# Kernel tuning notes

Measured on AMD Instinct MI355X. Metric: run time of the kernel, lower is better.

Reference implementation:

```python
import jax, jax.numpy as jnp
import numpy as np

B, T, S, H, D = 2, 2048, 2048, 16, 64
E = H * D  # embed_dim = 1024


def setup_inputs() -> dict:
    key = jax.random.key(0)
    k1, k2, k3, k4 = jax.random.split(key, 4)
    q = jax.random.normal(k1, (B, T, H, D), jnp.float32)
    kv = jax.random.normal(k2, (B, S, 2, H, D), jnp.float32)
    # nn.MultiheadAttention packed in-projection (xavier-ish scale) and out-projection
    in_proj_w = jax.random.normal(k3, (3 * E, E), jnp.float32) * (1.0 / np.sqrt(E)).astype(np.float32)
    in_proj_b = jnp.zeros((3 * E,), jnp.float32)
    out_proj_w = jax.random.normal(k4, (E, E), jnp.float32) * (1.0 / np.sqrt(E)).astype(np.float32)
    out_proj_b = jnp.zeros((E,), jnp.float32)
    return {"q": q, "kv": kv, "in_proj_w": in_proj_w, "in_proj_b": in_proj_b,
            "out_proj_w": out_proj_w, "out_proj_b": out_proj_b}


def reference(q, kv, in_proj_w, in_proj_b, out_proj_w, out_proj_b):
    Bq, Tq, Hh, Dd = q.shape
    Ss = kv.shape[1]
    Ee = Hh * Dd
    # flatten heads: q -> (B,T,E); kv unbinds k (two=0) and v (two=1)
    qf = q.reshape(Bq, Tq, Ee)
    kf = kv[:, :, 0].reshape(Bq, Ss, Ee)
    vf = kv[:, :, 1].reshape(Bq, Ss, Ee)
    wq, wk, wv = jnp.split(in_proj_w, 3, axis=0)
    bq, bk, bv = jnp.split(in_proj_b, 3)
    qp = (qf @ wq.T + bq).reshape(Bq, Tq, Hh, Dd).transpose(0, 2, 1, 3)  # bhtd
    kp = (kf @ wk.T + bk).reshape(Bq, Ss, Hh, Dd).transpose(0, 2, 1, 3)  # bhsd
    vp = (vf @ wv.T + bv).reshape(Bq, Ss, Hh, Dd).transpose(0, 2, 1, 3)  # bhsd
    scale = 1.0 / jnp.sqrt(jnp.asarray(Dd, qp.dtype))
    scores = jnp.einsum('bhtd,bhsd->bhts', qp, kp) * scale
    attn = jax.nn.softmax(scores, axis=-1)  # full SxS materialization, as in non-fused MHA
    ctx = jnp.einsum('bhts,bhsd->bhtd', attn, vp)
    ctx = ctx.transpose(0, 2, 1, 3).reshape(Bq, Tq, Ee)
    out = (ctx @ out_proj_w.T + out_proj_b).reshape(Bq, Tq, Hh, Dd)
    # need_weights=True default: weights averaged over heads -> (B,T,S)
    attn_weights = attn.mean(axis=1)
    return out, attn_weights
```

## Files before the change

kernel.cpp:

```cpp
#include <hip/hip_runtime.h>
#include <math.h>

#define Bb 2
#define Tt 2048
#define Ssz 2048
#define Hh 16
#define Dd 64
#define Ee 1024

#define NQ  (Bb*Tt*Ee)
#define NKV (Bb*Ssz*Ee)
#define NW  (3*Ee*Ee)
#define NWO (Ee*Ee)

#define LOG2E 1.44269504088896f

typedef __bf16 bf16x8 __attribute__((ext_vector_type(8)));
typedef float  floatx4 __attribute__((ext_vector_type(4)));
typedef unsigned short u16;
typedef unsigned int   u32;

__device__ __forceinline__ u16 f2bf(float f) {
    __bf16 h = (__bf16)f;
    union { __bf16 h; u16 u; } v; v.h = h; return v.u;
}
__device__ __forceinline__ float bf2f(u16 b) {
    union { u32 u; float f; } v; v.u = ((u32)b) << 16; return v.f;
}
__device__ __forceinline__ float load_f(const void* p, int i, bool isbf) {
    if (isbf) return bf2f(((const u16*)p)[i]);
    return ((const float*)p)[i];
}
__device__ __forceinline__ u32 load2(const void* p, int i, bool isbf) {
    if (isbf) return ((const u32*)p)[i >> 1];
    float2 f = ((const float2*)p)[i >> 1];
    return (u32)f2bf(f.x) | ((u32)f2bf(f.y) << 16);
}

typedef __attribute__((address_space(1))) const unsigned int gas_u32;
typedef __attribute__((address_space(3))) unsigned int las_u32;
__device__ __forceinline__ void gl_lds16(const u16* g, u16* l) {
    __builtin_amdgcn_global_load_lds((gas_u32*)g, (las_u32*)l, 16, 0, 0);
}

__device__ __forceinline__ int swz(int k, int row) {
    return (k & ~63) | ((((k >> 3) ^ row) & 7) << 3) | (k & 7);
}

__global__ void k_detect(const u32* __restrict__ qw, int* __restrict__ flag) {
    __shared__ int cnt;
    if (threadIdx.x == 0) cnt = 0;
    __syncthreads();
    int h = 0;
    for (int i = threadIdx.x; i < 4096; i += 256) {
        u32 w = qw[i];
        u32 b = (w >> 8) & 0x7Fu;
        if ((b & 0x7Cu) == 0x3Cu) h++;
    }
    atomicAdd(&cnt, h);
    __syncthreads();
    if (threadIdx.x == 0) flag[0] = (cnt > 2048) ? 1 : 0;
}

__global__ void k_pack(const void* __restrict__ q, const void* __restrict__ kv,
                       const void* __restrict__ w_in, const void* __restrict__ b_in,
                       const void* __restrict__ w_out, const void* __restrict__ b_out,
                       const int* __restrict__ flag,
                       u32* __restrict__ qb, u32* __restrict__ kb, u32* __restrict__ vb,
                       u32* __restrict__ wb, u32* __restrict__ wob, float* __restrict__ biases) {
    bool isbf = flag[0] != 0;
    int i = (blockIdx.x * 256 + threadIdx.x) * 2;
    if (i < NQ) { int row = i >> 10, k = i & 1023;
        qb[(((size_t)row << 10) | (u32)swz(k, row)) >> 1] = load2(q, i, isbf); return; }
    i -= NQ;
    if (i < NKV) { int row = i >> 10, e = i & 1023;
        kb[(((size_t)row << 10) | (u32)swz(e, row)) >> 1] = load2(kv, row*2048 + e, isbf); return; }
    i -= NKV;
    if (i < NKV) { int row = i >> 10, e = i & 1023;
        vb[(((size_t)row << 10) | (u32)swz(e, row)) >> 1] = load2(kv, row*2048 + 1024 + e, isbf); return; }
    i -= NKV;
    if (i < NW) { int row = i >> 10, k = i & 1023;
        wb[(((size_t)row << 10) | (u32)swz(k, row)) >> 1] = load2(w_in, i, isbf); return; }
    i -= NW;
    if (i < NWO) { int row = i >> 10, k = i & 1023;
        wob[(((size_t)row << 10) | (u32)swz(k, row)) >> 1] = load2(w_out, i, isbf); return; }
    i -= NWO;
    if (i < 3072) { biases[i] = load_f(b_in, i, isbf); biases[i+1] = load_f(b_in, i+1, isbf); return; }
    i -= 3072;
    if (i < 1024) { biases[3072+i] = load_f(b_out, i, isbf); biases[3072+i+1] = load_f(b_out, i+1, isbf); }
}

__device__ __forceinline__ void gemm128(const u16* __restrict__ Ab, const u16* __restrict__ Wb,
                                        u16* As, u16* Ws, floatx4 (&acc)[4][4], int tid) {
    int lane = tid & 63, w = tid >> 6, q = lane >> 4, ml = lane & 15;
    int mh = (w >> 1) * 64, nh = (w & 1) * 64;
    int rs = tid >> 3, cs = (tid & 7) * 8;
    for (int k0 = 0; k0 < 1024; k0 += 64) {
        __syncthreads();
#pragma unroll
        for (int j = 0; j < 4; ++j)
            gl_lds16(Ab + (size_t)(j*32 + rs) * 1024 + k0 + cs, &As[(j*32 + rs)*64 + cs]);
#pragma unroll
        for (int j = 0; j < 4; ++j)
            gl_lds16(Wb + (size_t)(j*32 + rs) * 1024 + k0 + cs, &Ws[(j*32 + rs)*64 + cs]);
        __syncthreads();
#pragma unroll
        for (int kk = 0; kk < 2; ++kk) {
            int gs = (((kk*4 + q) ^ ml) & 7) * 8;
            bf16x8 af[4], bfv[4];
#pragma unroll
            for (int mt = 0; mt < 4; ++mt) af[mt]  = *(const bf16x8*)&As[(mh + mt*16 + ml)*64 + gs];
#pragma unroll
            for (int nt = 0; nt < 4; ++nt) bfv[nt] = *(const bf16x8*)&Ws[(nh + nt*16 + ml)*64 + gs];
#pragma unroll
            for (int mt = 0; mt < 4; ++mt)
#pragma unroll
                for (int nt = 0; nt < 4; ++nt)
                    acc[mt][nt] = __builtin_amdgcn_mfma_f32_16x16x32_bf16(af[mt], bfv[nt], acc[mt][nt], 0, 0, 0);
        }
    }
}

__global__ __launch_bounds__(256) void k_gemm_qkv(const u16* __restrict__ qb, const u16* __restrict__ kb,
                                                  const u16* __restrict__ vb, const u16* __restrict__ wb,
                                                  const float* __restrict__ biases,
                                                  u16* __restrict__ Qp, u16* __restrict__ Kp,
                                                  u16* __restrict__ Vt) {
    __shared__ u16 As[128 * 64];
    __shared__ u16 Ws[128 * 64];
    int mode = blockIdx.z;
    const u16* A = (mode == 0) ? qb : (mode == 1) ? kb : vb;
    const u16* W = wb + (size_t)mode * Ee * Ee;
    const float* bias = biases + mode * 1024;
    int n0 = blockIdx.x * 128, m0 = blockIdx.y * 128;
    int tid = threadIdx.x, lane = tid & 63;
    int w = tid >> 6, q = lane >> 4, ml = lane & 15;
    int mh = (w >> 1) * 64, nh = (w & 1) * 64;

    floatx4 acc[4][4];
#pragma unroll
    for (int a = 0; a < 4; ++a)
#pragma unroll
        for (int b2 = 0; b2 < 4; ++b2) acc[a][b2] = (floatx4){0.f, 0.f, 0.f, 0.f};

    gemm128(A + (size_t)m0 * 1024, W + (size_t)n0 * 1024, As, Ws, acc, tid);

#pragma unroll
    for (int mt = 0; mt < 4; ++mt) {
#pragma unroll
        for (int nt = 0; nt < 4; ++nt) {
#pragma unroll
            for (int rg = 0; rg < 4; ++rg) {
                int m = m0 + mh + mt*16 + q*4 + rg;
                int n = n0 + nh + nt*16 + ml;
                float val = acc[mt][nt][rg] + bias[n];
                int b = m >> 11, t = m & 2047, hh = n >> 6, d = n & 63;
                if (mode == 0) {
                    int dsw = ((((d >> 3) ^ t) & 7) << 3) | (d & 7);
                    Qp[((size_t)(b*16 + hh) * 2048 + t) * 64 + dsw] = f2bf(val * (0.125f * LOG2E));
                } else if (mode == 1) {
                    int dsw = ((((d >> 3) ^ t) & 7) << 3) | (d & 7);
                    Kp[((size_t)(b*16 + hh) * 2048 + t) * 64 + dsw] = f2bf(val);
                } else {
                    int tsw = (t & ~63) | ((((t >> 3) ^ d) & 7) << 3) | (t & 7);
                    Vt[((size_t)(b*16 + hh) * 64 + d) * 2048 + tsw] = f2bf(val);
                }
            }
        }
    }
}

__global__ __launch_bounds__(256) void k_gemm_out(const u16* __restrict__ A, const u16* __restrict__ W,
                                                  const float* __restrict__ bias, void* __restrict__ Cout,
                                                  const int* __restrict__ flag) {
    __shared__ u16 As[128 * 64];
    __shared__ u16 Ws[128 * 64];
    int n0 = blockIdx.x * 128, m0 = blockIdx.y * 128;
    int tid = threadIdx.x, lane = tid & 63;
    int w = tid >> 6, q = lane >> 4, ml = lane & 15;
    int mh = (w >> 1) * 64, nh = (w & 1) * 64;

    floatx4 acc[4][4];
#pragma unroll
    for (int a = 0; a < 4; ++a)
#pragma unroll
        for (int b2 = 0; b2 < 4; ++b2) acc[a][b2] = (floatx4){0.f, 0.f, 0.f, 0.f};

    gemm128(A + (size_t)m0 * 1024, W + (size_t)n0 * 1024, As, Ws, acc, tid);

    bool outbf = flag[0] != 0;
#pragma unroll
    for (int mt = 0; mt < 4; ++mt) {
#pragma unroll
        for (int nt = 0; nt < 4; ++nt) {
#pragma unroll
            for (int rg = 0; rg < 4; ++rg) {
                int m = m0 + mh + mt*16 + q*4 + rg;
                int n = n0 + nh + nt*16 + ml;
                float val = acc[mt][nt][rg] + bias[n];
                if (outbf) ((u16*)Cout)[(size_t)m * 1024 + n] = f2bf(val);
                else       ((float*)Cout)[(size_t)m * 1024 + n] = val;
            }
        }
    }
}

__global__ __launch_bounds__(256) void k_flash(const u16* __restrict__ Qp, const u16* __restrict__ Kp,
                                               const u16* __restrict__ Vt, u16* __restrict__ ctx,
                                               float* __restrict__ lbuf) {
    __shared__ u16 Qs[128 * 64];
    __shared__ u16 Ks[64 * 64];
    __shared__ u16 Vs[64 * 64];
    __shared__ u16 Ps[128 * 64];
    int t0 = blockIdx.x * 128;
    int h  = blockIdx.y;
    int b  = blockIdx.z;
    const u16* Qh = Qp + (size_t)(b*16 + h) * 2048 * 64;
    const u16* Kh = Kp + (size_t)(b*16 + h) * 2048 * 64;
    const u16* Vh = Vt + (size_t)(b*16 + h) * 64 * 2048;
    int tid = threadIdx.x, lane = tid & 63;
    int w = tid >> 6, q = lane >> 4, ml = lane & 15;
    int rsw = tid >> 3, cs = (tid & 7) * 8;

#pragma unroll
    for (int j = 0; j < 4; ++j)
        gl_lds16(Qh + (size_t)(t0 + j*32 + rsw) * 64 + cs, &Qs[(j*32 + rsw)*64 + cs]);
    __syncthreads();

    bf16x8 qf[2][2];
#pragma unroll
    for (int mt = 0; mt < 2; ++mt)
#pragma unroll
        for (int kk = 0; kk < 2; ++kk)
            qf[mt][kk] = *(const bf16x8*)&Qs[(mt*64 + w*16 + ml)*64 + (((kk*4 + q) ^ ml) & 7)*8];

    float lp[2][4] = {{0.f,0.f,0.f,0.f},{0.f,0.f,0.f,0.f}};
    floatx4 ct[2][4];
#pragma unroll
    for (int mt = 0; mt < 2; ++mt)
#pragma unroll
        for (int i = 0; i < 4; ++i) ct[mt][i] = (floatx4){0.f, 0.f, 0.f, 0.f};

    for (int s0 = 0; s0 < 2048; s0 += 64) {
        __syncthreads();
#pragma unroll
        for (int j = 0; j < 2; ++j) {
            gl_lds16(Kh + (size_t)(s0 + j*32 + rsw) * 64 + cs, &Ks[(j*32 + rsw)*64 + cs]);
            gl_lds16(Vh + (size_t)(j*32 + rsw) * 2048 + s0 + cs, &Vs[(j*32 + rsw)*64 + cs]);
        }
        __syncthreads();

#pragma unroll
        for (int mt = 0; mt < 2; ++mt) {
            floatx4 sc[4];
#pragma unroll
            for (int i = 0; i < 4; ++i) sc[i] = (floatx4){0.f, 0.f, 0.f, 0.f};
#pragma unroll
            for (int kk = 0; kk < 2; ++kk) {
                int gs = (((kk*4 + q) ^ ml) & 7) * 8;
#pragma unroll
                for (int nt = 0; nt < 4; ++nt) {
                    bf16x8 kf = *(const bf16x8*)&Ks[(nt*16 + ml)*64 + gs];
                    sc[nt] = __builtin_amdgcn_mfma_f32_16x16x32_bf16(qf[mt][kk], kf, sc[nt], 0, 0, 0);
                }
            }
#pragma unroll
            for (int nt = 0; nt < 4; ++nt) {
#pragma unroll
                for (int rg = 0; rg < 4; ++rg) {
                    float p = __builtin_amdgcn_exp2f(sc[nt][rg]);
                    lp[mt][rg] += p;
                    int rr = q*4 + rg;
                    Ps[(mt*64 + w*16 + rr)*64 + (((nt*2 + (ml >> 3)) ^ rr) & 7)*8 + (ml & 7)] = f2bf(p);
                }
            }
        }

#pragma unroll
        for (int kk = 0; kk < 2; ++kk) {
            int gs = (((kk*4 + q) ^ ml) & 7) * 8;
            bf16x8 pf0 = *(const bf16x8*)&Ps[(w*16 + ml)*64 + gs];
            bf16x8 pf1 = *(const bf16x8*)&Ps[(64 + w*16 + ml)*64 + gs];
#pragma unroll
            for (int nt = 0; nt < 4; ++nt) {
                bf16x8 vf = *(const bf16x8*)&Vs[(nt*16 + ml)*64 + gs];
                ct[0][nt] = __builtin_amdgcn_mfma_f32_16x16x32_bf16(pf0, vf, ct[0][nt], 0, 0, 0);
                ct[1][nt] = __builtin_amdgcn_mfma_f32_16x16x32_bf16(pf1, vf, ct[1][nt], 0, 0, 0);
            }
        }
    }

#pragma unroll
    for (int mt = 0; mt < 2; ++mt)
#pragma unroll
        for (int rg = 0; rg < 4; ++rg)
#pragma unroll
            for (int off = 1; off < 16; off <<= 1) lp[mt][rg] += __shfl_xor(lp[mt][rg], off, 16);
    if (ml == 0) {
#pragma unroll
        for (int mt = 0; mt < 2; ++mt) {
            size_t base = (size_t)(b*16 + h) * 2048 + t0 + mt*64 + w*16 + q*4;
#pragma unroll
            for (int rg = 0; rg < 4; ++rg) lbuf[base + rg] = lp[mt][rg];
        }
    }

#pragma unroll
    for (int mt = 0; mt < 2; ++mt) {
        float il[4];
#pragma unroll
        for (int rg = 0; rg < 4; ++rg) il[rg] = 1.f / lp[mt][rg];
#pragma unroll
        for (int nt = 0; nt < 4; ++nt) {
#pragma unroll
            for (int rg = 0; rg < 4; ++rg) {
                int t = t0 + mt*64 + w*16 + q*4 + rg;
                int c64 = nt*16 + ml;
                int col = h*64 + (((((c64 >> 3) ^ t) & 7)) << 3) + (c64 & 7);
                ctx[(size_t)(b*2048 + t) * 1024 + col] = f2bf(ct[mt][nt][rg] * il[rg]);
            }
        }
    }
}

__global__ __launch_bounds__(256) void k_attnw(const u16* __restrict__ Qp, const u16* __restrict__ Kp,
                                               const float* __restrict__ lbuf,
                                               void* __restrict__ dout, const int* __restrict__ flag) {
    __shared__ u16 Qs[64 * 64];
    __shared__ u16 Ks[128 * 64];
    int s0 = blockIdx.x * 128;
    int t0 = blockIdx.y * 64;
    int b  = blockIdx.z;
    int tid = threadIdx.x, lane = tid & 63;
    int w = tid >> 6, q = lane >> 4, ml = lane & 15;
    int rsw = tid >> 3, cs = (tid & 7) * 8;

    floatx4 aw[8];
#pragma unroll
    for (int i = 0; i < 8; ++i) aw[i] = (floatx4){0.f, 0.f, 0.f, 0.f};

    for (int h = 0; h < 16; ++h) {
        const u16* Qh = Qp + (size_t)(b*16 + h) * 2048 * 64;
        const u16* Kh = Kp + (size_t)(b*16 + h) * 2048 * 64;
        __syncthreads();
#pragma unroll
        for (int j = 0; j < 2; ++j)
            gl_lds16(Qh + (size_t)(t0 + j*32 + rsw) * 64 + cs, &Qs[(j*32 + rsw)*64 + cs]);
#pragma unroll
        for (int j = 0; j < 4; ++j)
            gl_lds16(Kh + (size_t)(s0 + j*32 + rsw) * 64 + cs, &Ks[(j*32 + rsw)*64 + cs]);
        __syncthreads();

        float il[4];
        size_t sb = (size_t)(b*16 + h) * 2048 + t0 + w*16 + q*4;
#pragma unroll
        for (int rg = 0; rg < 4; ++rg) il[rg] = 1.f / lbuf[sb + rg];

        floatx4 sc[8];
#pragma unroll
        for (int i = 0; i < 8; ++i) sc[i] = (floatx4){0.f, 0.f, 0.f, 0.f};
#pragma unroll
        for (int kk = 0; kk < 2; ++kk) {
            int gs = (((kk*4 + q) ^ ml) & 7) * 8;
            bf16x8 qfr = *(const bf16x8*)&Qs[(w*16 + ml)*64 + gs];
#pragma unroll
            for (int nt = 0; nt < 8; ++nt) {
                bf16x8 kfr = *(const bf16x8*)&Ks[(nt*16 + ml)*64 + gs];
                sc[nt] = __builtin_amdgcn_mfma_f32_16x16x32_bf16(qfr, kfr, sc[nt], 0, 0, 0);
            }
        }
#pragma unroll
        for (int nt = 0; nt < 8; ++nt)
#pragma unroll
            for (int rg = 0; rg < 4; ++rg)
                aw[nt][rg] += __builtin_amdgcn_exp2f(sc[nt][rg]) * il[rg];
    }

    bool outbf = flag[0] != 0;
    const size_t attn_base = (size_t)Bb * Tt * Ee;
#pragma unroll
    for (int nt = 0; nt < 8; ++nt) {
#pragma unroll
        for (int rg = 0; rg < 4; ++rg) {
            int t = t0 + w*16 + q*4 + rg;
            int s = s0 + nt*16 + ml;
            float val = aw[nt][rg] * 0.0625f;
            size_t idx = attn_base + (size_t)(b*2048 + t) * 2048 + s;
            if (outbf) ((u16*)dout)[idx] = f2bf(val);
            else       ((float*)dout)[idx] = val;
        }
    }
}

extern "C" void kernel_launch(void* const* d_in, const int* in_sizes, int n_in,
                              void* d_out, int out_size, void* d_ws, size_t ws_size,
                              hipStream_t stream) {
    const void* q     = d_in[0];
    const void* kv    = d_in[1];
    const void* w_in  = d_in[2];
    const void* b_in  = d_in[3];
    const void* w_out = d_in[4];
    const void* b_out = d_in[5];

    char* ws = (char*)d_ws;
    size_t off = 0;
    auto alloc = [&](size_t bytes) -> void* {
        void* p = ws + off;
        off += (bytes + 255) & ~(size_t)255;
        return p;
    };
    int*   flag   = (int*)alloc(256);
    u16*   qb     = (u16*)alloc((size_t)NQ * 2);
    u16*   kb     = (u16*)alloc((size_t)NKV * 2);
    u16*   vb     = (u16*)alloc((size_t)NKV * 2);
    u16*   wb     = (u16*)alloc((size_t)NW * 2);
    u16*   wob    = (u16*)alloc((size_t)NWO * 2);
    float* biases = (float*)alloc(4096 * 4);
    u16*   Qp     = (u16*)alloc((size_t)NQ * 2);
    u16*   Kp     = (u16*)alloc((size_t)NKV * 2);
    u16*   Vt     = (u16*)alloc((size_t)NKV * 2);
    u16*   ctx    = (u16*)alloc((size_t)NQ * 2);
    float* lbuf   = (float*)alloc((size_t)Bb * Hh * Tt * 4);

    k_detect<<<1, 256, 0, stream>>>((const u32*)q, flag);

    int totalPairs = (NQ + NKV + NKV + NW + NWO + 4096) / 2;
    k_pack<<<(totalPairs + 255) / 256, 256, 0, stream>>>(q, kv, w_in, b_in, w_out, b_out, flag,
                                                         (u32*)qb, (u32*)kb, (u32*)vb,
                                                         (u32*)wb, (u32*)wob, biases);

    k_gemm_qkv<<<dim3(8, 32, 3), 256, 0, stream>>>(qb, kb, vb, wb, biases, Qp, Kp, Vt);

    k_flash<<<dim3(Tt / 128, Hh, Bb), 256, 0, stream>>>(Qp, Kp, Vt, ctx, lbuf);
    k_attnw<<<dim3(Ssz / 128, Tt / 64, Bb), 256, 0, stream>>>(Qp, Kp, lbuf, d_out, flag);

    k_gemm_out<<<dim3(8, 32), 256, 0, stream>>>(ctx, wob, biases + 3072, d_out, flag);
}
```

Baseline: 313.6 us.

## Software-pipeline flash attention loop with double-buffered K, V and P tiles

The flash kernel's KV loop is restructured so that K, V and P live in double-buffered shared memory. The QK^T and exp step for tile t+1 is interleaved with the PV product for tile t, and the global-to-LDS loads for upcoming tiles are issued ahead. This drops one barrier per iteration and overlaps load latency with MFMA work, at the cost of doubling LDS use (which may lower occupancy) and adding a prologue and epilogue.

```diff
diff --git a/kernel.cpp b/kernel.cpp
--- a/kernel.cpp
+++ b/kernel.cpp
@@ -209,9 +209,9 @@
                                                const u16* __restrict__ Vt, u16* __restrict__ ctx,
                                                float* __restrict__ lbuf) {
     __shared__ u16 Qs[128 * 64];
-    __shared__ u16 Ks[64 * 64];
-    __shared__ u16 Vs[64 * 64];
-    __shared__ u16 Ps[128 * 64];
+    __shared__ u16 Ks[2][64 * 64];
+    __shared__ u16 Vs[2][64 * 64];
+    __shared__ u16 Ps[2][128 * 64];
     int t0 = blockIdx.x * 128;
     int h  = blockIdx.y;
     int b  = blockIdx.z;
@@ -225,7 +225,16 @@
 #pragma unroll
     for (int j = 0; j < 4; ++j)
         gl_lds16(Qh + (size_t)(t0 + j*32 + rsw) * 64 + cs, &Qs[(j*32 + rsw)*64 + cs]);
+#pragma unroll
+    for (int j = 0; j < 2; ++j)
+        gl_lds16(Kh + (size_t)(j*32 + rsw) * 64 + cs, &Ks[0][(j*32 + rsw)*64 + cs]);
     __syncthreads();
+
+#pragma unroll
+    for (int j = 0; j < 2; ++j) {
+        gl_lds16(Kh + (size_t)(64 + j*32 + rsw) * 64 + cs, &Ks[1][(j*32 + rsw)*64 + cs]);
+        gl_lds16(Vh + (size_t)(j*32 + rsw) * 2048 + cs, &Vs[0][(j*32 + rsw)*64 + cs]);
+    }
 
     bf16x8 qf[2][2];
 #pragma unroll
@@ -241,52 +250,100 @@
 #pragma unroll
         for (int i = 0; i < 4; ++i) ct[mt][i] = (floatx4){0.f, 0.f, 0.f, 0.f};
 
-    for (int s0 = 0; s0 < 2048; s0 += 64) {
-        __syncthreads();
-#pragma unroll
-        for (int j = 0; j < 2; ++j) {
-            gl_lds16(Kh + (size_t)(s0 + j*32 + rsw) * 64 + cs, &Ks[(j*32 + rsw)*64 + cs]);
-            gl_lds16(Vh + (size_t)(j*32 + rsw) * 2048 + s0 + cs, &Vs[(j*32 + rsw)*64 + cs]);
-        }
-        __syncthreads();
-
+#pragma unroll
+    for (int mt = 0; mt < 2; ++mt) {
+        floatx4 sc[4];
+#pragma unroll
+        for (int i = 0; i < 4; ++i) sc[i] = (floatx4){0.f, 0.f, 0.f, 0.f};
+#pragma unroll
+        for (int kk = 0; kk < 2; ++kk) {
+            int gs = (((kk*4 + q) ^ ml) & 7) * 8;
+#pragma unroll
+            for (int nt = 0; nt < 4; ++nt) {
+                bf16x8 kf = *(const bf16x8*)&Ks[0][(nt*16 + ml)*64 + gs];
+                sc[nt] = __builtin_amdgcn_mfma_f32_16x16x32_bf16(qf[mt][kk], kf, sc[nt], 0, 0, 0);
+            }
+        }
+#pragma unroll
+        for (int nt = 0; nt < 4; ++nt) {
+#pragma unroll
+            for (int rg = 0; rg < 4; ++rg) {
+                float p = __builtin_amdgcn_exp2f(sc[nt][rg]);
+                lp[mt][rg] += p;
+                int rr = q*4 + rg;
+                Ps[0][(mt*64 + w*16 + rr)*64 + (((nt*2 + (ml >> 3)) ^ rr) & 7)*8 + (ml & 7)] = f2bf(p);
+            }
+        }
+    }
+    __syncthreads();
+
+    for (int t = 0; t < 31; ++t) {
+        int pb = t & 1;
+        if (t < 30) {
+#pragma unroll
+            for (int j = 0; j < 2; ++j)
+                gl_lds16(Kh + (size_t)((t+2)*64 + j*32 + rsw) * 64 + cs, &Ks[pb][(j*32 + rsw)*64 + cs]);
+        }
+#pragma unroll
+        for (int j = 0; j < 2; ++j)
+            gl_lds16(Vh + (size_t)(j*32 + rsw) * 2048 + (t+1)*64 + cs, &Vs[pb ^ 1][(j*32 + rsw)*64 + cs]);
+
+        floatx4 sc[2][4];
 #pragma unroll
         for (int mt = 0; mt < 2; ++mt) {
-            floatx4 sc[4];
-#pragma unroll
-            for (int i = 0; i < 4; ++i) sc[i] = (floatx4){0.f, 0.f, 0.f, 0.f};
+#pragma unroll
+            for (int i = 0; i < 4; ++i) sc[mt][i] = (floatx4){0.f, 0.f, 0.f, 0.f};
 #pragma unroll
             for (int kk = 0; kk < 2; ++kk) {
                 int gs = (((kk*4 + q) ^ ml) & 7) * 8;
 #pragma unroll
                 for (int nt = 0; nt < 4; ++nt) {
-                    bf16x8 kf = *(const bf16x8*)&Ks[(nt*16 + ml)*64 + gs];
-                    sc[nt] = __builtin_amdgcn_mfma_f32_16x16x32_bf16(qf[mt][kk], kf, sc[nt], 0, 0, 0);
+                    bf16x8 kf = *(const bf16x8*)&Ks[pb ^ 1][(nt*16 + ml)*64 + gs];
+                    sc[mt][nt] = __builtin_amdgcn_mfma_f32_16x16x32_bf16(qf[mt][kk], kf, sc[mt][nt], 0, 0, 0);
                 }
             }
+        }
+
+#pragma unroll
+        for (int kk = 0; kk < 2; ++kk) {
+            int gs = (((kk*4 + q) ^ ml) & 7) * 8;
+            bf16x8 pf0 = *(const bf16x8*)&Ps[pb][(w*16 + ml)*64 + gs];
+            bf16x8 pf1 = *(const bf16x8*)&Ps[pb][(64 + w*16 + ml)*64 + gs];
 #pragma unroll
             for (int nt = 0; nt < 4; ++nt) {
+                bf16x8 vf = *(const bf16x8*)&Vs[pb][(nt*16 + ml)*64 + gs];
+                ct[0][nt] = __builtin_amdgcn_mfma_f32_16x16x32_bf16(pf0, vf, ct[0][nt], 0, 0, 0);
+                ct[1][nt] = __builtin_amdgcn_mfma_f32_16x16x32_bf16(pf1, vf, ct[1][nt], 0, 0, 0);
+            }
+        }
+
+#pragma unroll
+        for (int mt = 0; mt < 2; ++mt) {
+#pragma unroll
+            for (int nt = 0; nt < 4; ++nt) {
 #pragma unroll
                 for (int rg = 0; rg < 4; ++rg) {
-                    float p = __builtin_amdgcn_exp2f(sc[nt][rg]);
+                    float p = __builtin_amdgcn_exp2f(sc[mt][nt][rg]);
                     lp[mt][rg] += p;
                     int rr = q*4 + rg;
-                    Ps[(mt*64 + w*16 + rr)*64 + (((nt*2 + (ml >> 3)) ^ rr) & 7)*8 + (ml & 7)] = f2bf(p);
+                    Ps[pb ^ 1][(mt*64 + w*16 + rr)*64 + (((nt*2 + (ml >> 3)) ^ rr) & 7)*8 + (ml & 7)] = f2bf(p);
                 }
             }
         }
 
-#pragma unroll
-        for (int kk = 0; kk < 2; ++kk) {
-            int gs = (((kk*4 + q) ^ ml) & 7) * 8;
-            bf16x8 pf0 = *(const bf16x8*)&Ps[(w*16 + ml)*64 + gs];
-            bf16x8 pf1 = *(const bf16x8*)&Ps[(64 + w*16 + ml)*64 + gs];
-#pragma unroll
-            for (int nt = 0; nt < 4; ++nt) {
-                bf16x8 vf = *(const bf16x8*)&Vs[(nt*16 + ml)*64 + gs];
-                ct[0][nt] = __builtin_amdgcn_mfma_f32_16x16x32_bf16(pf0, vf, ct[0][nt], 0, 0, 0);
-                ct[1][nt] = __builtin_amdgcn_mfma_f32_16x16x32_bf16(pf1, vf, ct[1][nt], 0, 0, 0);
-            }
+        __syncthreads();
+    }
+
+#pragma unroll
+    for (int kk = 0; kk < 2; ++kk) {
+        int gs = (((kk*4 + q) ^ ml) & 7) * 8;
+        bf16x8 pf0 = *(const bf16x8*)&Ps[1][(w*16 + ml)*64 + gs];
+        bf16x8 pf1 = *(const bf16x8*)&Ps[1][(64 + w*16 + ml)*64 + gs];
+#pragma unroll
+        for (int nt = 0; nt < 4; ++nt) {
+            bf16x8 vf = *(const bf16x8*)&Vs[1][(nt*16 + ml)*64 + gs];
+            ct[0][nt] = __builtin_amdgcn_mfma_f32_16x16x32_bf16(pf0, vf, ct[0][nt], 0, 0, 0);
+            ct[1][nt] = __builtin_amdgcn_mfma_f32_16x16x32_bf16(pf1, vf, ct[1][nt], 0, 0, 0);
         }
     }
 
```

Measured after the change: 302.3 us. -3.6%, faster.

## Double-buffer K/V in flash kernel and use eight waves of 16 rows

Applied to the files above, without the earlier changes.

The flash-attention kernel now runs 512 threads per block, so each of eight waves owns 16 query rows instead of four waves owning 32. K and V tiles are double-buffered in shared memory. The next tile is prefetched with async global-to-LDS loads while the current tile is computed, which cuts the two barriers per iteration to one. The aim is to hide global load latency and raise wave-level parallelism, at the cost of more shared memory and a larger block that may lower the number of resident blocks.

```diff
diff --git a/kernel.cpp b/kernel.cpp
--- a/kernel.cpp
+++ b/kernel.cpp
@@ -205,12 +205,12 @@
     }
 }
 
-__global__ __launch_bounds__(256) void k_flash(const u16* __restrict__ Qp, const u16* __restrict__ Kp,
+__global__ __launch_bounds__(512) void k_flash(const u16* __restrict__ Qp, const u16* __restrict__ Kp,
                                                const u16* __restrict__ Vt, u16* __restrict__ ctx,
                                                float* __restrict__ lbuf) {
     __shared__ u16 Qs[128 * 64];
-    __shared__ u16 Ks[64 * 64];
-    __shared__ u16 Vs[64 * 64];
+    __shared__ u16 Ks[2][64 * 64];
+    __shared__ u16 Vs[2][64 * 64];
     __shared__ u16 Ps[128 * 64];
     int t0 = blockIdx.x * 128;
     int h  = blockIdx.y;
@@ -223,102 +223,91 @@
     int rsw = tid >> 3, cs = (tid & 7) * 8;
 
 #pragma unroll
-    for (int j = 0; j < 4; ++j)
-        gl_lds16(Qh + (size_t)(t0 + j*32 + rsw) * 64 + cs, &Qs[(j*32 + rsw)*64 + cs]);
+    for (int j = 0; j < 2; ++j)
+        gl_lds16(Qh + (size_t)(t0 + j*64 + rsw) * 64 + cs, &Qs[(j*64 + rsw)*64 + cs]);
+    gl_lds16(Kh + (size_t)rsw * 64 + cs, &Ks[0][rsw*64 + cs]);
+    gl_lds16(Vh + (size_t)rsw * 2048 + cs, &Vs[0][rsw*64 + cs]);
     __syncthreads();
 
-    bf16x8 qf[2][2];
-#pragma unroll
-    for (int mt = 0; mt < 2; ++mt)
-#pragma unroll
-        for (int kk = 0; kk < 2; ++kk)
-            qf[mt][kk] = *(const bf16x8*)&Qs[(mt*64 + w*16 + ml)*64 + (((kk*4 + q) ^ ml) & 7)*8];
-
-    float lp[2][4] = {{0.f,0.f,0.f,0.f},{0.f,0.f,0.f,0.f}};
-    floatx4 ct[2][4];
-#pragma unroll
-    for (int mt = 0; mt < 2; ++mt)
-#pragma unroll
-        for (int i = 0; i < 4; ++i) ct[mt][i] = (floatx4){0.f, 0.f, 0.f, 0.f};
-
+    bf16x8 qf[2];
+#pragma unroll
+    for (int kk = 0; kk < 2; ++kk)
+        qf[kk] = *(const bf16x8*)&Qs[(w*16 + ml)*64 + (((kk*4 + q) ^ ml) & 7)*8];
+
+    float lp[4] = {0.f, 0.f, 0.f, 0.f};
+    floatx4 ct[4];
+#pragma unroll
+    for (int i = 0; i < 4; ++i) ct[i] = (floatx4){0.f, 0.f, 0.f, 0.f};
+
+    int cur = 0;
     for (int s0 = 0; s0 < 2048; s0 += 64) {
-        __syncthreads();
-#pragma unroll
-        for (int j = 0; j < 2; ++j) {
-            gl_lds16(Kh + (size_t)(s0 + j*32 + rsw) * 64 + cs, &Ks[(j*32 + rsw)*64 + cs]);
-            gl_lds16(Vh + (size_t)(j*32 + rsw) * 2048 + s0 + cs, &Vs[(j*32 + rsw)*64 + cs]);
-        }
-        __syncthreads();
-
-#pragma unroll
-        for (int mt = 0; mt < 2; ++mt) {
-            floatx4 sc[4];
-#pragma unroll
-            for (int i = 0; i < 4; ++i) sc[i] = (floatx4){0.f, 0.f, 0.f, 0.f};
-#pragma unroll
-            for (int kk = 0; kk < 2; ++kk) {
-                int gs = (((kk*4 + q) ^ ml) & 7) * 8;
-#pragma unroll
-                for (int nt = 0; nt < 4; ++nt) {
-                    bf16x8 kf = *(const bf16x8*)&Ks[(nt*16 + ml)*64 + gs];
-                    sc[nt] = __builtin_amdgcn_mfma_f32_16x16x32_bf16(qf[mt][kk], kf, sc[nt], 0, 0, 0);
-                }
-            }
-#pragma unroll
-            for (int nt = 0; nt < 4; ++nt) {
-#pragma unroll
-                for (int rg = 0; rg < 4; ++rg) {
-                    float p = __builtin_amdgcn_exp2f(sc[nt][rg]);
-                    lp[mt][rg] += p;
-                    int rr = q*4 + rg;
-                    Ps[(mt*64 + w*16 + rr)*64 + (((nt*2 + (ml >> 3)) ^ rr) & 7)*8 + (ml & 7)] = f2bf(p);
-                }
-            }
-        }
-
+        if (s0 + 64 < 2048) {
+            gl_lds16(Kh + (size_t)(s0 + 64 + rsw) * 64 + cs, &Ks[cur ^ 1][rsw*64 + cs]);
+            gl_lds16(Vh + (size_t)rsw * 2048 + (s0 + 64) + cs, &Vs[cur ^ 1][rsw*64 + cs]);
+        }
+        const u16* Ksc = Ks[cur];
+        const u16* Vsc = Vs[cur];
+
+        floatx4 sc[4];
+#pragma unroll
+        for (int i = 0; i < 4; ++i) sc[i] = (floatx4){0.f, 0.f, 0.f, 0.f};
 #pragma unroll
         for (int kk = 0; kk < 2; ++kk) {
             int gs = (((kk*4 + q) ^ ml) & 7) * 8;
-            bf16x8 pf0 = *(const bf16x8*)&Ps[(w*16 + ml)*64 + gs];
-            bf16x8 pf1 = *(const bf16x8*)&Ps[(64 + w*16 + ml)*64 + gs];
 #pragma unroll
             for (int nt = 0; nt < 4; ++nt) {
-                bf16x8 vf = *(const bf16x8*)&Vs[(nt*16 + ml)*64 + gs];
-                ct[0][nt] = __builtin_amdgcn_mfma_f32_16x16x32_bf16(pf0, vf, ct[0][nt], 0, 0, 0);
-                ct[1][nt] = __builtin_amdgcn_mfma_f32_16x16x32_bf16(pf1, vf, ct[1][nt], 0, 0, 0);
-            }
-        }
-    }
-
-#pragma unroll
-    for (int mt = 0; mt < 2; ++mt)
-#pragma unroll
-        for (int rg = 0; rg < 4; ++rg)
-#pragma unroll
-            for (int off = 1; off < 16; off <<= 1) lp[mt][rg] += __shfl_xor(lp[mt][rg], off, 16);
+                bf16x8 kf = *(const bf16x8*)&Ksc[(nt*16 + ml)*64 + gs];
+                sc[nt] = __builtin_amdgcn_mfma_f32_16x16x32_bf16(qf[kk], kf, sc[nt], 0, 0, 0);
+            }
+        }
+
+#pragma unroll
+        for (int nt = 0; nt < 4; ++nt) {
+#pragma unroll
+            for (int rg = 0; rg < 4; ++rg) {
+                float p = __builtin_amdgcn_exp2f(sc[nt][rg]);
+                lp[rg] += p;
+                int rr = q*4 + rg;
+                Ps[(w*16 + rr)*64 + (((nt*2 + (ml >> 3)) ^ rr) & 7)*8 + (ml & 7)] = f2bf(p);
+            }
+        }
+
+#pragma unroll
+        for (int kk = 0; kk < 2; ++kk) {
+            int gs = (((kk*4 + q) ^ ml) & 7) * 8;
+            bf16x8 pf = *(const bf16x8*)&Ps[(w*16 + ml)*64 + gs];
+#pragma unroll
+            for (int nt = 0; nt < 4; ++nt) {
+                bf16x8 vf = *(const bf16x8*)&Vsc[(nt*16 + ml)*64 + gs];
+                ct[nt] = __builtin_amdgcn_mfma_f32_16x16x32_bf16(pf, vf, ct[nt], 0, 0, 0);
+            }
+        }
+
+        __syncthreads();
+        cur ^= 1;
+    }
+
+#pragma unroll
+    for (int rg = 0; rg < 4; ++rg)
+#pragma unroll
+        for (int off = 1; off < 16; off <<= 1) lp[rg] += __shfl_xor(lp[rg], off, 16);
     if (ml == 0) {
-#pragma unroll
-        for (int mt = 0; mt < 2; ++mt) {
-            size_t base = (size_t)(b*16 + h) * 2048 + t0 + mt*64 + w*16 + q*4;
-#pragma unroll
-            for (int rg = 0; rg < 4; ++rg) lbuf[base + rg] = lp[mt][rg];
-        }
-    }
-
-#pragma unroll
-    for (int mt = 0; mt < 2; ++mt) {
-        float il[4];
-#pragma unroll
-        for (int rg = 0; rg < 4; ++rg) il[rg] = 1.f / lp[mt][rg];
-#pragma unroll
-        for (int nt = 0; nt < 4; ++nt) {
-#pragma unroll
-            for (int rg = 0; rg < 4; ++rg) {
-                int t = t0 + mt*64 + w*16 + q*4 + rg;
-                int c64 = nt*16 + ml;
-                int col = h*64 + (((((c64 >> 3) ^ t) & 7)) << 3) + (c64 & 7);
-                ctx[(size_t)(b*2048 + t) * 1024 + col] = f2bf(ct[mt][nt][rg] * il[rg]);
-            }
+        size_t base = (size_t)(b*16 + h) * 2048 + t0 + w*16 + q*4;
+#pragma unroll
+        for (int rg = 0; rg < 4; ++rg) lbuf[base + rg] = lp[rg];
+    }
+
+    float il[4];
+#pragma unroll
+    for (int rg = 0; rg < 4; ++rg) il[rg] = 1.f / lp[rg];
+#pragma unroll
+    for (int nt = 0; nt < 4; ++nt) {
+#pragma unroll
+        for (int rg = 0; rg < 4; ++rg) {
+            int t = t0 + w*16 + q*4 + rg;
+            int c64 = nt*16 + ml;
+            int col = h*64 + (((((c64 >> 3) ^ t) & 7)) << 3) + (c64 & 7);
+            ctx[(size_t)(b*2048 + t) * 1024 + col] = f2bf(ct[nt][rg] * il[rg]);
         }
     }
 }
@@ -431,7 +420,7 @@
 
     k_gemm_qkv<<<dim3(8, 32, 3), 256, 0, stream>>>(qb, kb, vb, wb, biases, Qp, Kp, Vt);
 
-    k_flash<<<dim3(Tt / 128, Hh, Bb), 256, 0, stream>>>(Qp, Kp, Vt, ctx, lbuf);
+    k_flash<<<dim3(Tt / 128, Hh, Bb), 512, 0, stream>>>(Qp, Kp, Vt, ctx, lbuf);
     k_attnw<<<dim3(Ssz / 128, Tt / 64, Bb), 256, 0, stream>>>(Qp, Kp, lbuf, d_out, flag);
 
     k_gemm_out<<<dim3(8, 32), 256, 0, stream>>>(ctx, wob, biases + 3072, d_out, flag);
```

Result: faster. 289.3 us (-7.8%).
